# Kernel optimization log

Hardware: AMD Instinct MI355X
Metric: run time of the kernel (lower is better)

## Reference

```python
import jax, jax.numpy as jnp
import numpy as np

DIM = 768
NUM_HEADS = 12
HEAD_DIM = DIM // NUM_HEADS
SCALE = HEAD_DIM ** -0.5
EPS = 1e-6


def setup_inputs() -> dict:
    key = jax.random.key(0)
    k_x, k_p, k_qkv, k_proj = jax.random.split(key, 4)
    B, N = 16, 577
    x = jax.random.normal(k_x, (B, N, DIM), dtype=jnp.float32)
    # binary keep/drop policy per token (as produced by an upstream gumbel gate)
    policy = jax.random.randint(k_p, (B, N, 1), 0, 2).astype(jnp.float32)
    Wqkv = jax.random.normal(k_qkv, (DIM, 3 * DIM), dtype=jnp.float32) * 0.02
    bqkv = jnp.zeros((3 * DIM,), dtype=jnp.float32)
    Wproj = jax.random.normal(k_proj, (DIM, DIM), dtype=jnp.float32) * 0.02
    bproj = jnp.zeros((DIM,), dtype=jnp.float32)
    return {"x": x, "policy": policy, "Wqkv": Wqkv, "bqkv": bqkv,
            "Wproj": Wproj, "bproj": bproj}


def reference(x, policy, Wqkv, bqkv, Wproj, bproj):
    B, N, C = x.shape
    # qkv projection -> [3, B, H, N, Dh]
    qkv = (x @ Wqkv + bqkv).reshape(B, N, 3, NUM_HEADS, HEAD_DIM)
    qkv = jnp.transpose(qkv, (2, 0, 3, 1, 4))
    q, k, v = qkv[0], qkv[1], qkv[2]
    # scaled attention logits [B, H, N, N]
    attn = jnp.einsum("bhnd,bhmd->bhnm", q, k) * SCALE
    # policy-masked softmax (training-mode formula: eye keeps self-attention alive)
    ap = policy.reshape(B, 1, 1, N)
    eye = jnp.eye(N, dtype=ap.dtype).reshape(1, 1, N, N)
    ap = ap + (1.0 - ap) * eye
    max_att = jnp.max(attn, axis=-1, keepdims=True)
    e = jnp.exp(attn - max_att) * ap
    attn = (e + EPS / N) / (jnp.sum(e, axis=-1, keepdims=True) + EPS)
    # attend and project
    out = jnp.einsum("bhnm,bhmd->bhnd", attn, v)
    out = jnp.transpose(out, (0, 2, 1, 3)).reshape(B, N, C)
    return out @ Wproj + bproj
```

## Files before the change

kernel.cpp:

```cpp
#include <hip/hip_runtime.h>
#include <hip/hip_bf16.h>

#define QKVC   2304
#define NHEAD  12
#define NTOK   577
#define NBATCH 16
#define NROWS  (NBATCH * NTOK)
#define NPAD   640
#define SCALE  0.125f
#define EPSV   1e-6f
#define KT     24
#define CH     512
#define EXPC   0.18033688011f

typedef __bf16  bf16x8 __attribute__((ext_vector_type(8)));
typedef float   f32x4  __attribute__((ext_vector_type(4)));

__device__ __forceinline__ unsigned short f2bf(float f) {
    union { float f; unsigned u; } v; v.f = f;
    unsigned r = v.u + 0x7FFFu + ((v.u >> 16) & 1u);
    return (unsigned short)(r >> 16);
}
__device__ __forceinline__ unsigned short f2bf_trunc(float f) {
    return (unsigned short)(__float_as_uint(f) >> 16);
}
__device__ __forceinline__ unsigned pack2bf(float a, float b) {
    return (unsigned)f2bf(a) | ((unsigned)f2bf(b) << 16);
}
__device__ __forceinline__ f32x4 mfma16(bf16x8 a, bf16x8 b, f32x4 c) {
    return __builtin_amdgcn_mfma_f32_16x16x32_bf16(a, b, c, 0, 0, 0);
}

#define GLDS16(g, l) __builtin_amdgcn_global_load_lds( \
    (const __attribute__((address_space(1))) unsigned int*)(g), \
    (__attribute__((address_space(3))) unsigned int*)(l), 16, 0, 0)


__device__ void transpose_tile(const float* __restrict__ src, unsigned short* __restrict__ dst,
                               int N, int bx, int by, int t) {
    __shared__ unsigned short lt[64 * 72];
    int n0 = bx * 64, k0 = by * 64;
    int kk = t >> 4, nn = (t & 15) * 4;
    for (int i = 0; i < 4; i++) {
        int kr = kk + i * 16;
        float4 v = *(const float4*)&src[(size_t)(k0 + kr) * N + n0 + nn];
        lt[(nn + 0) * 72 + kr] = f2bf(v.x);
        lt[(nn + 1) * 72 + kr] = f2bf(v.y);
        lt[(nn + 2) * 72 + kr] = f2bf(v.z);
        lt[(nn + 3) * 72 + kr] = f2bf(v.w);
    }
    __syncthreads();
    int n = t >> 2;
    int ks = (t & 3) * 16;
    int gn = n0 + n;
    int ntile = gn >> 4, r = gn & 15, s = (r >> 1) & 3;
    for (int j = 0; j < 2; j++) {
        int k = k0 + ks + j * 8;
        int kt = k >> 5;
        int q = ((k >> 3) & 3) ^ s;
        uint4 v = *(uint4*)&lt[n * 72 + ks + j * 8];
        *(uint4*)&dst[((size_t)ntile * KT + kt) * CH + r * 32 + q * 8] = v;
    }
}

#define NCHUNK (577 * KT)
#define CONVB  ((NCHUNK + 15) / 16)
__global__ void k_prep(const float* __restrict__ x, unsigned short* __restrict__ xbt,
                       const float* __restrict__ Wqkv, unsigned short* __restrict__ wqkvt,
                       const float* __restrict__ Wproj, unsigned short* __restrict__ wprojt,
                       unsigned short* __restrict__ ktc, unsigned short* __restrict__ vtc) {
    int id = blockIdx.x, t = threadIdx.x;
    if (id < CONVB) {
        int cid = id * 16 + (t >> 4);
        if (cid < NCHUNK) {
            int r = t & 15;
            int mt = cid / KT, kt = cid - mt * KT;
            const float* src = x + ((size_t)mt * 16 + r) * 768 + kt * 32;
            int s = (r >> 1) & 3;
            unsigned short* dst = xbt + (size_t)cid * CH + r * 32;
            #pragma unroll
            for (int q = 0; q < 4; q++) {
                int g = q ^ s;
                float4 v0 = *(const float4*)(src + g * 8);
                float4 v1 = *(const float4*)(src + g * 8 + 4);
                uint4 u;
                u.x = pack2bf(v0.x, v0.y);
                u.y = pack2bf(v0.z, v0.w);
                u.z = pack2bf(v1.x, v1.y);
                u.w = pack2bf(v1.z, v1.w);
                *(uint4*)(dst + q * 8) = u;
            }
        }
    } else if (id < CONVB + 432) {
        int i2 = id - CONVB;
        transpose_tile(Wqkv, wqkvt, QKVC, i2 % 36, i2 / 36, t);
    } else if (id < CONVB + 432 + 144) {
        int i2 = id - CONVB - 432;
        transpose_tile(Wproj, wprojt, 768, i2 % 12, i2 / 12, t);
    } else {
        int bh = id - CONVB - 576;
        size_t base = (size_t)bh * 40960 + 36864;
        uint4 z = {0u, 0u, 0u, 0u};
        for (int i = t; i < 512; i += 256) {
            *(uint4*)&ktc[base + (size_t)i * 8] = z;
            *(uint4*)&vtc[base + (size_t)i * 8] = z;
        }
    }
}

template <bool F32OUT>
__global__ __launch_bounds__(512, 2)
void k_gemm(const unsigned short* __restrict__ A, const unsigned short* __restrict__ B,
            const float* __restrict__ bias, void* __restrict__ outp, int Ncols,
            unsigned short* __restrict__ ktp, unsigned short* __restrict__ vtp) {
    __shared__ unsigned short SL[36864];
    int t = threadIdx.x;
    int lane = t & 63, wave = t >> 6, quad = lane >> 4, l15 = lane & 15;
    int wm = wave >> 2, wn = wave & 3;
    int nT = Ncols >> 7;
    int nwg = gridDim.x;

    int q8 = nwg >> 3, r8 = nwg & 7;
    int xcd = blockIdx.x & 7, idx = blockIdx.x >> 3;
    int wg = (xcd < r8 ? xcd * (q8 + 1) : r8 * (q8 + 1) + (xcd - r8) * q8) + idx;
    int m0 = (wg / nT) * 256;
    int n0 = (wg % nT) * 128;

    const unsigned short* gA0 = A + ((size_t)((m0 >> 4) + wave) * KT) * CH + lane * 8;
    const unsigned short* gA1 = gA0 + (size_t)8 * KT * CH;
    const unsigned short* gB0 = B + ((size_t)((n0 >> 4) + wave) * KT) * CH + lane * 8;

    f32x4 acc[8][2] = {};

    auto STAGE = [&](int sx, unsigned slot) {
        unsigned sa = slot * 8192u + (unsigned)wave * 512u;
        unsigned sb = 24576u + slot * 4096u + (unsigned)wave * 512u;
        GLDS16(gA0 + sx * CH, &SL[sa]);
        GLDS16(gA1 + sx * CH, &SL[sa + 4096]);
        GLDS16(gB0 + sx * CH, &SL[sb]);
    };

    auto STEP = [&](unsigned slot, int sx, unsigned sslot, bool stage) {
        unsigned ab = slot * 8192u;
        unsigned bb = 24576u + slot * 4096u;
        unsigned ro = (unsigned)(quad ^ ((l15 >> 1) & 3)) * 8u;
        bf16x8 af[8], bfr[2];
        #pragma unroll
        for (int i = 0; i < 8; i++)
            af[i]  = *(const bf16x8*)&SL[ab + (unsigned)(wm * 128 + i * 16 + l15) * 32u + ro];
        #pragma unroll
        for (int i = 0; i < 2; i++)
            bfr[i] = *(const bf16x8*)&SL[bb + (unsigned)(wn * 32 + i * 16 + l15) * 32u + ro];
        if (stage) STAGE(sx, sslot);
        asm volatile("s_waitcnt lgkmcnt(0)" ::: "memory");
        __builtin_amdgcn_s_setprio(1);
        #pragma unroll
        for (int mi = 0; mi < 8; mi++)
            #pragma unroll
            for (int ni = 0; ni < 2; ni++)
                acc[mi][ni] = mfma16(af[mi], bfr[ni], acc[mi][ni]);
        __builtin_amdgcn_s_setprio(0);
    };

    STAGE(0, 0); STAGE(1, 1);
    for (int s = 0; s < 23; s++) {
        asm volatile("s_waitcnt vmcnt(3)" ::: "memory");
        asm volatile("s_barrier" ::: "memory");
        STEP((unsigned)(s % 3), s + 2, (unsigned)((s + 2) % 3), s < 22);
    }
    asm volatile("s_waitcnt vmcnt(0)" ::: "memory");
    asm volatile("s_barrier" ::: "memory");
    STEP(2u, 0, 0u, false);

    if constexpr (F32OUT) {
        for (int ni = 0; ni < 2; ni++) {
            int col = n0 + wn * 32 + ni * 16 + l15;
            float bv = bias[col];
            for (int mi = 0; mi < 8; mi++) {
                int rowm = m0 + wm * 128 + mi * 16 + quad * 4;
                for (int r = 0; r < 4; r++) {
                    int m = rowm + r;
                    if (m < NROWS)
                        ((float*)outp)[(size_t)m * Ncols + col] = acc[mi][ni][r] + bv;
                }
            }
        }
    } else {
        __syncthreads();
        for (int ni = 0; ni < 2; ni++) {
            int colL = wn * 32 + ni * 16 + l15;
            float bv = bias[n0 + colL];
            for (int mi = 0; mi < 8; mi++) {
                int rowL = wm * 128 + mi * 16 + quad * 4;
                for (int r = 0; r < 4; r++)
                    SL[(rowL + r) * 136 + colL] = f2bf(acc[mi][ni][r] + bv);
            }
        }
        __syncthreads();
        if (n0 < 768) {
            for (int rr = 0; rr < 8; rr++) {
                int row = rr * 32 + (t >> 4);
                int m = m0 + row;
                if (m < NROWS) {
                    uint4 v = *(uint4*)&SL[row * 136 + (t & 15) * 8];
                    *(uint4*)&((unsigned short*)outp)[(size_t)m * 768 + n0 + (t & 15) * 8] = v;
                }
            }
        } else if (n0 < 1536) {
            int cseg = (t & 15) * 8;
            int h = ((n0 - 768) >> 6) + (cseg >> 6);
            int d = cseg & 63;
            int dh = d >> 5, q = (d >> 3) & 3;
            for (int rr = 0; rr < 8; rr++) {
                int row = rr * 32 + (t >> 4);
                int m = m0 + row;
                if (m < NROWS) {
                    unsigned bbx = (unsigned)m / 577u;
                    int tok = m - (int)bbx * 577;
                    int r16 = tok & 15, s = (r16 >> 1) & 3;
                    uint4 v = *(uint4*)&SL[row * 136 + cseg];
                    *(uint4*)&ktp[((((size_t)bbx * NHEAD + h) * 40 + (tok >> 4)) * 2 + dh) * 512
                                  + r16 * 32 + (q ^ s) * 8] = v;
                }
            }
        } else {
            int h0 = (n0 - 1536) >> 6;
            for (int i = 0; i < 16; i++) {
                int c = wave * 16 + i;
                int h = h0 + (c >> 6), d = c & 63;
                int dt = d >> 4, r = d & 15, sr = (r >> 1) & 3;
                for (int half = 0; half < 4; half++) {
                    int lr = half * 64 + lane;
                    int m = m0 + lr;
                    if (m < NROWS) {
                        unsigned bbx = (unsigned)m / 577u;
                        int tok = m - (int)bbx * 577;
                        int tb = tok >> 6, kh = (tok >> 5) & 1, k32 = tok & 31;
                        int q = ((k32 >> 3) & 3) ^ sr;
                        vtp[((((size_t)bbx * NHEAD + h) * 10 + tb) * 8 + dt * 2 + kh) * 512
                            + r * 32 + q * 8 + (k32 & 7)] = SL[lr * 136 + c];
                    }
                }
            }
        }
    }
}

__global__ __launch_bounds__(256, 3)
void k_attn(const unsigned short* __restrict__ Qb, const unsigned short* __restrict__ ktc,
            const unsigned short* __restrict__ vtc,
            const float* __restrict__ policy, unsigned short* __restrict__ ao) {
    __shared__ unsigned short Kb[2][4096];
    __shared__ unsigned short Vb[2][4096];
    __shared__ unsigned short Ps[4][32 * 72];
    __shared__ float pol[NPAD];
    int t = threadIdx.x;
    int lane = t & 63, wave = t >> 6, quad = lane >> 4, l15 = lane & 15;
    int wg = (blockIdx.x & 7) * 120 + (blockIdx.x >> 3);
    int qt = wg % 5, bh = wg / 5;
    int h = bh % NHEAD, b = bh / NHEAD;
    const unsigned short* qbase = Qb + (size_t)(b * NTOK) * 768 + h * 64;
    const unsigned short* kcb = ktc + (size_t)bh * 40960 + lane * 8;
    const unsigned short* vcb = vtc + (size_t)bh * 40960 + lane * 8;

    for (int i = t; i < NPAD; i += 256)
        pol[i] = (i < NTOK) ? policy[b * NTOK + i] : 0.f;

    bf16x8 qf[2][2];
    for (int mi = 0; mi < 2; mi++) {
        const unsigned short* qp =
            qbase + (size_t)(qt * 128 + mi * 64 + wave * 16 + l15) * 768 + quad * 8;
        qf[mi][0] = *(const bf16x8*)qp;
        qf[mi][1] = *(const bf16x8*)(qp + 32);
    }
    bf16x8 onesf;
    for (int j = 0; j < 8; j++) onesf[j] = (__bf16)1.0f;
    f32x4 o[2][4] = {};
    f32x4 ls[2] = {};
    int rowtok0[2];
    for (int mi = 0; mi < 2; mi++)
        rowtok0[mi] = qt * 128 + mi * 64 + wave * 16 + quad * 4;

    auto STAGEA = [&](int kt) {
        int buf = kt & 1;
        GLDS16(kcb + ((size_t)(kt * 4 + wave) * 2 + 0) * 512, &Kb[buf][(wave * 2 + 0) * 512]);
        GLDS16(kcb + ((size_t)(kt * 4 + wave) * 2 + 1) * 512, &Kb[buf][(wave * 2 + 1) * 512]);
        GLDS16(vcb + ((size_t)(kt * 8 + wave * 2 + 0)) * 512, &Vb[buf][(wave * 2 + 0) * 512]);
        GLDS16(vcb + ((size_t)(kt * 8 + wave * 2 + 1)) * 512, &Vb[buf][(wave * 2 + 1) * 512]);
    };

    STAGEA(0);
    __syncthreads();

    for (int kt = 0; kt < 10; kt++) {
        if (kt) {
            asm volatile("s_waitcnt vmcnt(0)" ::: "memory");
            asm volatile("s_barrier" ::: "memory");
        }
        if (kt < 9) STAGEA(kt + 1);
        const unsigned short* KB = &Kb[kt & 1][0];
        const unsigned short* VB = &Vb[kt & 1][0];
        unsigned ro = (unsigned)(quad ^ ((l15 >> 1) & 3)) * 8u;
        int key0 = kt * 64;

        for (int ci = 0; ci < 4; ci++) {
            bf16x8 kf0 = *(const bf16x8*)&KB[(ci * 2 + 0) * 512 + l15 * 32 + ro];
            bf16x8 kf1 = *(const bf16x8*)&KB[(ci * 2 + 1) * 512 + l15 * 32 + ro];
            int col = key0 + ci * 16 + l15;
            float pc = pol[col];
            for (int mi = 0; mi < 2; mi++) {
                f32x4 a = {};
                a = mfma16(qf[mi][0], kf0, a);
                a = mfma16(qf[mi][1], kf1, a);
                for (int r = 0; r < 4; r++) {
                    float ap = (col == rowtok0[mi] + r) ? 1.f : pc;
                    float e = __builtin_amdgcn_exp2f(a[r] * EXPC) * ap;
                    Ps[wave][(mi * 16 + quad * 4 + r) * 72 + ci * 16 + l15] = f2bf_trunc(e);
                }
            }
        }
        __asm__ volatile("s_waitcnt lgkmcnt(0)" ::: "memory");
        bf16x8 pf[2][2];
        for (int mi = 0; mi < 2; mi++) {
            pf[mi][0] = *(const bf16x8*)&Ps[wave][(mi * 16 + l15) * 72 + quad * 8];
            pf[mi][1] = *(const bf16x8*)&Ps[wave][(mi * 16 + l15) * 72 + 32 + quad * 8];
            ls[mi] = mfma16(pf[mi][0], onesf, ls[mi]);
            ls[mi] = mfma16(pf[mi][1], onesf, ls[mi]);
        }
        for (int di = 0; di < 4; di++) {
            bf16x8 vf0 = *(const bf16x8*)&VB[(di * 2 + 0) * 512 + l15 * 32 + ro];
            bf16x8 vf1 = *(const bf16x8*)&VB[(di * 2 + 1) * 512 + l15 * 32 + ro];
            for (int mi = 0; mi < 2; mi++) {
                o[mi][di] = mfma16(pf[mi][0], vf0, o[mi][di]);
                o[mi][di] = mfma16(pf[mi][1], vf1, o[mi][di]);
            }
        }
    }

    for (int mi = 0; mi < 2; mi++) {
        for (int r = 0; r < 4; r++) {
            int tok = rowtok0[mi] + r;
            if (tok < NTOK) {
                float inv = __builtin_amdgcn_rcpf(ls[mi][r] + EPSV);
                int m = b * NTOK + tok;
                int mt = m >> 4, rr = m & 15, s = (rr >> 1) & 3;
                unsigned short* dst = ao + ((size_t)mt * KT) * CH + rr * 32;
                for (int di = 0; di < 4; di++) {
                    int k = h * 64 + di * 16 + l15;
                    int kt2 = k >> 5;
                    int q = ((k >> 3) & 3) ^ s;
                    dst[(size_t)kt2 * CH + q * 8 + (l15 & 7)] =
                        f2bf(o[mi][di][r] * inv);
                }
            }
        }
    }
}

extern "C" void kernel_launch(void* const* d_in, const int* in_sizes, int n_in,
                              void* d_out, int out_size, void* d_ws, size_t ws_size,
                              hipStream_t stream) {
    const float* x      = (const float*)d_in[0];
    const float* policy = (const float*)d_in[1];
    const float* Wqkv   = (const float*)d_in[2];
    const float* bqkv   = (const float*)d_in[3];
    const float* Wproj  = (const float*)d_in[4];
    const float* bproj  = (const float*)d_in[5];
    float* out = (float*)d_out;

    unsigned short* p = (unsigned short*)d_ws;
    unsigned short* xb     = p;
    unsigned short* ao     = p; p += (size_t)NROWS * 768;
    unsigned short* wqkvt  = p; p += (size_t)QKVC * 768;
    unsigned short* wprojt = p; p += (size_t)768 * 768;
    unsigned short* Qb     = p; p += (size_t)NROWS * 768;
    unsigned short* ktc    = p; p += (size_t)NBATCH * NHEAD * 40960;
    unsigned short* vtc    = p; p += (size_t)NBATCH * NHEAD * 40960;

    int mT = (NROWS + 255) / 256;

    k_prep<<<CONVB + 432 + 144 + 192, 256, 0, stream>>>(
        x, xb, Wqkv, wqkvt, Wproj, wprojt, ktc, vtc);
    k_gemm<false><<<mT * (QKVC / 128), 512, 0, stream>>>(
        xb, wqkvt, bqkv, (void*)Qb, QKVC, ktc, vtc);
    k_attn<<<NPAD / 128 * NHEAD * NBATCH, 256, 0, stream>>>(
        Qb, ktc, vtc, policy, ao);
    k_gemm<true><<<mT * (768 / 128), 512, 0, stream>>>(
        ao, wprojt, bproj, (void*)out, 768, nullptr, nullptr);
}
```

Measured before the change: 193.0 us.

## Load V fragments directly from global into registers, drop V LDS staging

The V tensor is rewritten by the QKV kernel in a lane-contiguous fragment layout, so each lane in the attention kernel can fetch its MFMA B-operand straight from global memory as 16-byte loads. The V double buffer in shared memory is removed, which cuts LDS footprint, and launch bounds are raised from 3 to 4 waves per EU to allow more occupancy. V loads are now issued each iteration without being prefetched a tile ahead, so their latency may be exposed, and the extra register pressure could cause spills under the tighter occupancy target.

```diff
diff --git a/kernel.cpp b/kernel.cpp
--- a/kernel.cpp
+++ b/kernel.cpp
@@ -228,17 +228,17 @@
             for (int i = 0; i < 16; i++) {
                 int c = wave * 16 + i;
                 int h = h0 + (c >> 6), d = c & 63;
-                int dt = d >> 4, r = d & 15, sr = (r >> 1) & 3;
-                for (int half = 0; half < 4; half++) {
-                    int lr = half * 64 + lane;
+                int di = d >> 4, l15v = d & 15;
+                for (int half4 = 0; half4 < 4; half4++) {
+                    int lr = half4 * 64 + lane;
                     int m = m0 + lr;
                     if (m < NROWS) {
                         unsigned bbx = (unsigned)m / 577u;
                         int tok = m - (int)bbx * 577;
-                        int tb = tok >> 6, kh = (tok >> 5) & 1, k32 = tok & 31;
-                        int q = ((k32 >> 3) & 3) ^ sr;
-                        vtp[((((size_t)bbx * NHEAD + h) * 10 + tb) * 8 + dt * 2 + kh) * 512
-                            + r * 32 + q * 8 + (k32 & 7)] = SL[lr * 136 + c];
+                        vtp[((size_t)bbx * NHEAD + h) * 40960
+                            + (((tok >> 6) * 4 + di) * 2 + ((tok >> 5) & 1)) * 512
+                            + ((((tok >> 3) & 3) * 16 + l15v)) * 8 + (tok & 7)]
+                            = SL[lr * 136 + c];
                     }
                 }
             }
@@ -246,12 +246,11 @@
     }
 }
 
-__global__ __launch_bounds__(256, 3)
+__global__ __launch_bounds__(256, 4)
 void k_attn(const unsigned short* __restrict__ Qb, const unsigned short* __restrict__ ktc,
             const unsigned short* __restrict__ vtc,
             const float* __restrict__ policy, unsigned short* __restrict__ ao) {
     __shared__ unsigned short Kb[2][4096];
-    __shared__ unsigned short Vb[2][4096];
     __shared__ unsigned short Ps[4][32 * 72];
     __shared__ float pol[NPAD];
     int t = threadIdx.x;
@@ -281,15 +280,13 @@
     for (int mi = 0; mi < 2; mi++)
         rowtok0[mi] = qt * 128 + mi * 64 + wave * 16 + quad * 4;
 
-    auto STAGEA = [&](int kt) {
+    auto STAGEK = [&](int kt) {
         int buf = kt & 1;
         GLDS16(kcb + ((size_t)(kt * 4 + wave) * 2 + 0) * 512, &Kb[buf][(wave * 2 + 0) * 512]);
         GLDS16(kcb + ((size_t)(kt * 4 + wave) * 2 + 1) * 512, &Kb[buf][(wave * 2 + 1) * 512]);
-        GLDS16(vcb + ((size_t)(kt * 8 + wave * 2 + 0)) * 512, &Vb[buf][(wave * 2 + 0) * 512]);
-        GLDS16(vcb + ((size_t)(kt * 8 + wave * 2 + 1)) * 512, &Vb[buf][(wave * 2 + 1) * 512]);
     };
 
-    STAGEA(0);
+    STAGEK(0);
     __syncthreads();
 
     for (int kt = 0; kt < 10; kt++) {
@@ -297,9 +294,13 @@
             asm volatile("s_waitcnt vmcnt(0)" ::: "memory");
             asm volatile("s_barrier" ::: "memory");
         }
-        if (kt < 9) STAGEA(kt + 1);
+        const unsigned short* vks = vcb + (size_t)kt * 4096;
+        bf16x8 vf[8];
+        #pragma unroll
+        for (int j = 0; j < 8; j++)
+            vf[j] = *(const bf16x8*)(vks + j * 512);
+        if (kt < 9) STAGEK(kt + 1);
         const unsigned short* KB = &Kb[kt & 1][0];
-        const unsigned short* VB = &Vb[kt & 1][0];
         unsigned ro = (unsigned)(quad ^ ((l15 >> 1) & 3)) * 8u;
         int key0 = kt * 64;
 
@@ -328,11 +329,9 @@
             ls[mi] = mfma16(pf[mi][1], onesf, ls[mi]);
         }
         for (int di = 0; di < 4; di++) {
-            bf16x8 vf0 = *(const bf16x8*)&VB[(di * 2 + 0) * 512 + l15 * 32 + ro];
-            bf16x8 vf1 = *(const bf16x8*)&VB[(di * 2 + 1) * 512 + l15 * 32 + ro];
             for (int mi = 0; mi < 2; mi++) {
-                o[mi][di] = mfma16(pf[mi][0], vf0, o[mi][di]);
-                o[mi][di] = mfma16(pf[mi][1], vf1, o[mi][di]);
+                o[mi][di] = mfma16(pf[mi][0], vf[di * 2 + 0], o[mi][di]);
+                o[mi][di] = mfma16(pf[mi][1], vf[di * 2 + 1], o[mi][di]);
             }
         }
     }
```

Measured after the change: 198.7 us. +2.9%, slower.
